# Optimization experiments

Measured on AMD Instinct MI355X. Metric: run time of the kernel, lower is better.

## Reference

```python
import jax, jax.numpy as jnp
import numpy as np

DIM, HEADS, DIM_HEAD = 1024, 16, 64
INNER = HEADS * DIM_HEAD  # 1024
FF = 4 * DIM
EPS = 1e-5


def layer_norm(x, g, b):
    mu = jnp.mean(x, axis=-1, keepdims=True)
    var = jnp.mean(jnp.square(x - mu), axis=-1, keepdims=True)
    return (x - mu) * jax.lax.rsqrt(var + EPS) * g + b


def setup_inputs() -> dict:
    key = jax.random.key(0)
    ks = jax.random.split(key, 8)
    B, N = 2, 2048
    s = 0.02
    return {
        "x": jax.random.normal(ks[0], (B, N, DIM), dtype=jnp.float32),
        "ln1_g": jnp.ones((DIM,), jnp.float32),
        "ln1_b": jnp.zeros((DIM,), jnp.float32),
        "ln2_g": jnp.ones((DIM,), jnp.float32),
        "ln2_b": jnp.zeros((DIM,), jnp.float32),
        "w_qkv": jax.random.normal(ks[1], (DIM, 3 * INNER), jnp.float32) * s,
        "w_out": jax.random.normal(ks[2], (INNER, DIM), jnp.float32) * s,
        "b_out": jnp.zeros((DIM,), jnp.float32),
        "w_ff1": jax.random.normal(ks[3], (DIM, FF), jnp.float32) * s,
        "b_ff1": jnp.zeros((FF,), jnp.float32),
        "w_ff2": jax.random.normal(ks[4], (FF, DIM), jnp.float32) * s,
        "b_ff2": jnp.zeros((DIM,), jnp.float32),
    }


def reference(x, ln1_g, ln1_b, ln2_g, ln2_b, w_qkv, w_out, b_out,
              w_ff1, b_ff1, w_ff2, b_ff2):
    B, N, _ = x.shape
    scale = DIM_HEAD ** -0.5
    h = layer_norm(x, ln1_g, ln1_b)
    qkv = h @ w_qkv  # [B, N, 3*INNER]
    q, k, v = jnp.split(qkv, 3, axis=-1)
    # b n (h d) -> b h n d
    def to_heads(t):
        return t.reshape(B, N, HEADS, DIM_HEAD).transpose(0, 2, 1, 3)
    q, k, v = to_heads(q), to_heads(k), to_heads(v)
    dots = jnp.einsum('bhnd,bhmd->bhnm', q, k) * scale
    attn = jax.nn.softmax(dots, axis=-1)  # dropout = identity (eval)
    out = jnp.einsum('bhnm,bhmd->bhnd', attn, v)
    out = out.transpose(0, 2, 1, 3).reshape(B, N, INNER)
    out = out @ w_out + b_out
    x = x + out  # residual
    h2 = layer_norm(x, ln2_g, ln2_b)
    ff = jax.nn.gelu(h2 @ w_ff1 + b_ff1, approximate=False) @ w_ff2 + b_ff2
    return x + ff
```

## Files before the change

kernel.cpp:

```cpp
#include <hip/hip_runtime.h>
#include <hip/hip_bf16.h>
#include <math.h>

#define SEQ   2048
#define BATCH 2
#define NROWS 4096
#define DIMM  1024
#define QKV3  3072
#define FFD   4096
#define NHEAD 16
#define DHEAD 64

typedef __bf16 bf16;
typedef __bf16 bf16x4 __attribute__((ext_vector_type(4)));
typedef __bf16 bf16x8 __attribute__((ext_vector_type(8)));
typedef float  f32x4  __attribute__((ext_vector_type(4)));

static __device__ __forceinline__ f32x4 mfma16(bf16x8 a, bf16x8 b, f32x4 c) {
    return __builtin_amdgcn_mfma_f32_16x16x32_bf16(a, b, c, 0, 0, 0);
}

#define GLDS16(gp, lp) __builtin_amdgcn_global_load_lds( \
    (__attribute__((address_space(1))) void*)(gp),       \
    (__attribute__((address_space(3))) void*)(lp), 16, 0, 0)

__global__ __launch_bounds__(256) void tcast_kernel(
    const float* __restrict__ src, bf16* __restrict__ dst, int K, int N)
{
    __shared__ float tile[32][33];
    const int n0 = blockIdx.x * 32;
    const int k0 = blockIdx.y * 32;
    const int r = threadIdx.x >> 5;
    const int c = threadIdx.x & 31;
    #pragma unroll
    for (int i = 0; i < 4; ++i)
        tile[r + 8 * i][c] = src[(size_t)(k0 + r + 8 * i) * N + n0 + c];
    __syncthreads();
    #pragma unroll
    for (int i = 0; i < 4; ++i)
        dst[(size_t)(n0 + r + 8 * i) * K + k0 + c] = (bf16)tile[c][r + 8 * i];
}

__global__ __launch_bounds__(256) void ln_cast_kernel(
    const float* __restrict__ x, const float* __restrict__ g,
    const float* __restrict__ b, bf16* __restrict__ out)
{
    const int row = blockIdx.x;
    const int t = threadIdx.x;
    const float4 v = ((const float4*)(x + (size_t)row * DIMM))[t];
    float s  = v.x + v.y + v.z + v.w;
    float sq = v.x * v.x + v.y * v.y + v.z * v.z + v.w * v.w;
    #pragma unroll
    for (int m = 1; m < 64; m <<= 1) {
        s  += __shfl_xor(s, m, 64);
        sq += __shfl_xor(sq, m, 64);
    }
    __shared__ float ss[4], ssq[4];
    const int wave = t >> 6;
    if ((t & 63) == 0) { ss[wave] = s; ssq[wave] = sq; }
    __syncthreads();
    s  = ss[0] + ss[1] + ss[2] + ss[3];
    sq = ssq[0] + ssq[1] + ssq[2] + ssq[3];
    const float mean = s * (1.0f / DIMM);
    const float var  = sq * (1.0f / DIMM) - mean * mean;
    const float rs   = rsqrtf(var + 1e-5f);
    const float4 gv = ((const float4*)g)[t];
    const float4 bv = ((const float4*)b)[t];
    bf16* o = out + (size_t)row * DIMM + t * 4;
    o[0] = (bf16)((v.x - mean) * rs * gv.x + bv.x);
    o[1] = (bf16)((v.y - mean) * rs * gv.y + bv.y);
    o[2] = (bf16)((v.z - mean) * rs * gv.z + bv.z);
    o[3] = (bf16)((v.w - mean) * rs * gv.w + bv.w);
}

template<int EPI>
__global__ __launch_bounds__(512, 2)
void gemm256_kernel(const bf16* __restrict__ A, const bf16* __restrict__ BT,
                    const float* __restrict__ bias, bf16* __restrict__ C,
                    int M, int N, int K, int ld)
{
    __shared__ bf16 As_[2][2][8192];
    __shared__ bf16 Bs_[2][2][8192];
    const int nb = N >> 8;
    const int chunk = (int)gridDim.x >> 3;
    const int idx = ((int)blockIdx.x & 7) * chunk + ((int)blockIdx.x >> 3);
    const int bm = idx / nb, bn = idx - bm * nb;
    const int tm = bm << 8, tn = bn << 8;
    const int tid = threadIdx.x;
    const int lane = tid & 63, w = tid >> 6;
    const int wr = w >> 2, wc = w & 3;
    const int lq = lane & 15, hk = lane >> 4;

    const int sr  = lane >> 3;
    const int sgo = (((lane & 7) ^ sr) << 3);
    const bf16* gA0 = A  + (size_t)(tm +       w * 8 + sr) * ld + sgo;
    const bf16* gA1 = A  + (size_t)(tm + 128 + w * 8 + sr) * ld + sgo;
    const bf16* gB0 = BT + (size_t)(tn +       w * 8 + sr) * ld + sgo;
    const bf16* gB1 = BT + (size_t)(tn + 128 + w * 8 + sr) * ld + sgo;
    const size_t l64 = (size_t)64 * ld;

#define STG(D, T) do {                                                   \
        const size_t ko_ = (size_t)(T) * 64;                             \
        GLDS16(gA0 + ko_,       &As_[D][0][w * 512]);                    \
        GLDS16(gA0 + ko_ + l64, &As_[D][0][4096 + w * 512]);             \
        GLDS16(gA1 + ko_,       &As_[D][1][w * 512]);                    \
        GLDS16(gA1 + ko_ + l64, &As_[D][1][4096 + w * 512]);             \
        GLDS16(gB0 + ko_,       &Bs_[D][0][w * 512]);                    \
        GLDS16(gB0 + ko_ + l64, &Bs_[D][0][4096 + w * 512]);             \
        GLDS16(gB1 + ko_,       &Bs_[D][1][w * 512]);                    \
        GLDS16(gB1 + ko_ + l64, &Bs_[D][1][4096 + w * 512]);             \
    } while (0)

    f32x4 acc[8][4] = {};

    const int NT = K >> 6;
    STG(0, 0);
    STG(1, 1);
    for (int t = 0; t < NT; ++t) {
        const int d = t & 1;
        if (t + 1 < NT) asm volatile("s_waitcnt vmcnt(8)" ::: "memory");
        else            asm volatile("s_waitcnt vmcnt(0)" ::: "memory");
        __builtin_amdgcn_s_barrier();

        const char* Ah = (const char*)&As_[d][wr][0];
        const char* Bh = (const char*)&Bs_[d][wc >> 1][0];

        bf16x8 bfv[4][2];
        #pragma unroll
        for (int nj = 0; nj < 4; ++nj) {
            const int lc = (wc & 1) * 64 + nj * 16 + lq;
            #pragma unroll
            for (int kk = 0; kk < 2; ++kk) {
                const int g = kk * 4 + hk;
                bfv[nj][kk] = *(const bf16x8*)(Bh + lc * 128 + ((g ^ (lc & 7)) << 4));
            }
        }
        #pragma unroll
        for (int half = 0; half < 2; ++half) {
            bf16x8 af[4][2];
            #pragma unroll
            for (int mi = 0; mi < 4; ++mi) {
                const int lr = (half * 4 + mi) * 16 + lq;
                #pragma unroll
                for (int kk = 0; kk < 2; ++kk) {
                    const int g = kk * 4 + hk;
                    af[mi][kk] = *(const bf16x8*)(Ah + lr * 128 + ((g ^ (lr & 7)) << 4));
                }
            }
            __builtin_amdgcn_s_setprio(1);
            #pragma unroll
            for (int mi = 0; mi < 4; ++mi)
                #pragma unroll
                for (int nj = 0; nj < 4; ++nj)
                    #pragma unroll
                    for (int kk = 0; kk < 2; ++kk)
                        acc[half * 4 + mi][nj] =
                            mfma16(bfv[nj][kk], af[mi][kk], acc[half * 4 + mi][nj]);
            __builtin_amdgcn_s_setprio(0);
        }

        asm volatile("" ::: "memory");
        __builtin_amdgcn_s_barrier();
        if (t + 2 < NT) STG(d, t + 2);
    }
#undef STG

    const int r0 = tm + wr * 128 + lq;
    const int c0 = tn + wc * 64 + (hk << 2);
    if (EPI == 0) {
        #pragma unroll
        for (int mi = 0; mi < 8; ++mi)
            #pragma unroll
            for (int nj = 0; nj < 4; ++nj) {
                bf16x4 pk = { (bf16)acc[mi][nj][0], (bf16)acc[mi][nj][1],
                              (bf16)acc[mi][nj][2], (bf16)acc[mi][nj][3] };
                *(bf16x4*)(C + (size_t)(r0 + mi * 16) * N + c0 + nj * 16) = pk;
            }
    } else {
        #pragma unroll
        for (int nj = 0; nj < 4; ++nj) {
            const float4 bv4 = *(const float4*)(bias + c0 + nj * 16);
            #pragma unroll
            for (int mi = 0; mi < 8; ++mi) {
                float v0 = acc[mi][nj][0] + bv4.x, v1 = acc[mi][nj][1] + bv4.y;
                float v2 = acc[mi][nj][2] + bv4.z, v3 = acc[mi][nj][3] + bv4.w;
                bf16x4 pk = {
                    (bf16)(0.5f * v0 * (1.0f + erff(v0 * 0.70710678118654752f))),
                    (bf16)(0.5f * v1 * (1.0f + erff(v1 * 0.70710678118654752f))),
                    (bf16)(0.5f * v2 * (1.0f + erff(v2 * 0.70710678118654752f))),
                    (bf16)(0.5f * v3 * (1.0f + erff(v3 * 0.70710678118654752f))) };
                *(bf16x4*)(C + (size_t)(r0 + mi * 16) * N + c0 + nj * 16) = pk;
            }
        }
    }
}

template<int EPI>
__global__ __launch_bounds__(256, 3)
void gemm_bt_kernel(const bf16* __restrict__ A, const bf16* __restrict__ BT,
                    const float* __restrict__ bias, const float* __restrict__ res,
                    void* __restrict__ Cout, int M, int N, int K, int ld)
{
    __shared__ bf16 As[3][4096];
    __shared__ bf16 Bs[3][4096];
    const int nb = N >> 7;
    const int chunk = (int)gridDim.x >> 3;
    int idx = (blockIdx.x & 7) * chunk + (blockIdx.x >> 3);
    int ks = 0;
    if (EPI == 3) {
        const int tiles = (M >> 7) * nb;
        ks = idx / tiles;
        idx -= ks * tiles;
    }
    const int bm = idx / nb, bn = idx - bm * nb;
    const int tm = bm << 7, tn = bn << 7;
    const int tid = threadIdx.x;
    const int lane = tid & 63, wave = tid >> 6;
    const int wm = (wave >> 1) << 6, wn = (wave & 1) << 6;
    const int kofs = ks * K;

    const bf16* ga = A  + (size_t)(tm + wave * 32 + (lane >> 2)) * ld + kofs + ((lane & 3) << 3);
    const bf16* gb = BT + (size_t)(tn + wave * 32 + (lane >> 2)) * ld + kofs + ((lane & 3) << 3);
    const size_t k16 = (size_t)16 * ld;

    f32x4 acc[4][4] = {};
    const int ro = (lane & 15) * 32 + ((lane >> 4) << 3);

#define GSTAGE(BUF, KO) do {                          \
        bf16* la_ = &As[BUF][wave * 1024];            \
        bf16* lb_ = &Bs[BUF][wave * 1024];            \
        GLDS16(ga + (KO),       la_);                 \
        GLDS16(ga + (KO) + k16, la_ + 512);           \
        GLDS16(gb + (KO),       lb_);                 \
        GLDS16(gb + (KO) + k16, lb_ + 512);           \
    } while (0)

    GSTAGE(0, 0);
    GSTAGE(1, 32);
    GSTAGE(2, 64);
    int cur = 0;
    for (int k0 = 0; k0 < K; k0 += 32) {
        if (k0 + 96 <= K)      asm volatile("s_waitcnt vmcnt(8)" ::: "memory");
        else if (k0 + 64 <= K) asm volatile("s_waitcnt vmcnt(4)" ::: "memory");
        else                   asm volatile("s_waitcnt vmcnt(0)" ::: "memory");
        __builtin_amdgcn_s_barrier();

        bf16x8 af[4], bfr[4];
        #pragma unroll
        for (int i = 0; i < 4; ++i) {
            af[i]  = *(const bf16x8*)(&As[cur][0] + (wm + i * 16) * 32 + ro);
            bfr[i] = *(const bf16x8*)(&Bs[cur][0] + (wn + i * 16) * 32 + ro);
        }
        #pragma unroll
        for (int i = 0; i < 4; ++i)
            #pragma unroll
            for (int j = 0; j < 4; ++j)
                acc[i][j] = mfma16(bfr[j], af[i], acc[i][j]);

        asm volatile("" ::: "memory");
        __builtin_amdgcn_s_barrier();
        asm volatile("" ::: "memory");
        if (k0 + 96 < K) GSTAGE(cur, k0 + 96);
        cur = (cur == 2) ? 0 : cur + 1;
    }
#undef GSTAGE

    const int lq = lane & 15, hk = lane >> 4;
    const int r0 = tm + wm + lq;
    const int c0 = tn + wn + (hk << 2);
    if (EPI == 1) {
        float* C = (float*)Cout;
        #pragma unroll
        for (int j = 0; j < 4; ++j) {
            const float4 bv4 = *(const float4*)(bias + c0 + j * 16);
            #pragma unroll
            for (int i = 0; i < 4; ++i) {
                const size_t off = (size_t)(r0 + i * 16) * N + c0 + j * 16;
                const float4 rv = *(const float4*)(res + off);
                float4 o;
                o.x = acc[i][j][0] + bv4.x + rv.x;
                o.y = acc[i][j][1] + bv4.y + rv.y;
                o.z = acc[i][j][2] + bv4.z + rv.z;
                o.w = acc[i][j][3] + bv4.w + rv.w;
                *(float4*)(C + off) = o;
            }
        }
    } else {
        float* C = (float*)(ks == 0 ? Cout : (void*)res);
        #pragma unroll
        for (int j = 0; j < 4; ++j)
            #pragma unroll
            for (int i = 0; i < 4; ++i) {
                float4 o = { acc[i][j][0], acc[i][j][1], acc[i][j][2], acc[i][j][3] };
                *(float4*)(C + (size_t)(r0 + i * 16) * N + c0 + j * 16) = o;
            }
    }
}

__global__ __launch_bounds__(256) void ff2_reduce_kernel(
    const float* __restrict__ p0, const float* __restrict__ p1,
    const float* __restrict__ bias, const float* __restrict__ res,
    float* __restrict__ out)
{
    const int i = blockIdx.x * 256 + threadIdx.x;
    const float4 a = ((const float4*)p0)[i];
    const float4 b = ((const float4*)p1)[i];
    const float4 r = ((const float4*)res)[i];
    const float4 g = ((const float4*)bias)[i & 255];
    float4 o;
    o.x = a.x + b.x + r.x + g.x;
    o.y = a.y + b.y + r.y + g.y;
    o.z = a.z + b.z + r.z + g.z;
    o.w = a.w + b.w + r.w + g.w;
    ((float4*)out)[i] = o;
}

__global__ __launch_bounds__(256) void vtrans_kernel(
    const bf16* __restrict__ qkv, bf16* __restrict__ vT)
{
    __shared__ bf16 t[64 * 64];
    const int n0 = blockIdx.x * 64;
    const int bh = blockIdx.y;
    const int b = bh >> 4, h = bh & 15;
    const bf16* src = qkv + (size_t)(b * SEQ + n0) * QKV3 + 2 * DIMM + h * DHEAD;

    #pragma unroll
    for (int it = 0; it < 2; ++it) {
        const int c = it * 256 + threadIdx.x;
        const int n = c >> 3, d8 = (c & 7) * 8;
        const bf16x8 v8 = *(const bf16x8*)(src + (size_t)n * QKV3 + d8);
        const int byte = (n * 128 + d8 * 2) ^ (((n >> 3) & 7) << 4);
        *(bf16x8*)((char*)t + byte) = v8;
    }
    __syncthreads();
    #pragma unroll
    for (int it = 0; it < 2; ++it) {
        const int c = it * 256 + threadIdx.x;
        const int d = c >> 3, nc = c & 7;
        bf16x8 o8;
        #pragma unroll
        for (int i = 0; i < 8; ++i) {
            const int n = nc * 8 + i;
            const int byte = (n * 128 + d * 2) ^ ((nc & 7) << 4);
            o8[i] = *(const bf16*)((const char*)t + byte);
        }
        *(bf16x8*)(vT + (size_t)bh * DHEAD * SEQ + (size_t)d * SEQ + n0 + nc * 8) = o8;
    }
}

__global__ __launch_bounds__(256, 4)
void attn_kernel(const bf16* __restrict__ qkv, const bf16* __restrict__ vT,
                 bf16* __restrict__ out)
{
    __shared__ bf16 Ks[2][64 * 64];
    __shared__ bf16 Vs[2][64 * 64];
    __shared__ bf16 Ps[4][16 * 64];
    const int bid = blockIdx.x;
    const int idx = (bid & 7) * 128 + (bid >> 3);
    const int qt = idx & 31;
    const int bh = idx >> 5;
    const int b = bh >> 4, h = bh & 15;
    const int tid = threadIdx.x;
    const int lane = tid & 63, wave = tid >> 6;
    const int q = lane & 15, hi = lane >> 4;

    const bf16* qbase = qkv + (size_t)(b * SEQ) * QKV3 + h * DHEAD;
    const bf16* kbase = qbase + DIMM;
    const bf16* vbase = vT + (size_t)bh * DHEAD * SEQ;

    const int q0 = qt * 64 + wave * 16;
    bf16x8 qf[2];
    {
        const bf16* qp = qbase + (size_t)(q0 + q) * QKV3 + (hi << 3);
        qf[0] = *(const bf16x8*)qp;
        qf[1] = *(const bf16x8*)(qp + 32);
        #pragma unroll
        for (int j = 0; j < 8; ++j) {
            qf[0][j] = (bf16)((float)qf[0][j] * 0.125f);
            qf[1][j] = (bf16)((float)qf[1][j] * 0.125f);
        }
    }

    const int srow = lane >> 3;
    const int scol = ((lane & 7) ^ srow) << 3;
    const bf16* gk = kbase + (size_t)(wave * 16 + srow) * QKV3 + scol;
    const bf16* gv = vbase + (size_t)(wave * 16 + srow) * SEQ + scol;

#define STAGE(BUF, KT) do {                                        \
        bf16* lk_ = &Ks[BUF][wave * 1024];                         \
        bf16* lv_ = &Vs[BUF][wave * 1024];                         \
        GLDS16(gk + (size_t)(KT) * QKV3,       lk_);               \
        GLDS16(gk + (size_t)((KT) + 8) * QKV3, lk_ + 512);         \
        GLDS16(gv + (KT),                      lv_);               \
        GLDS16(gv + (KT) + 8 * SEQ,            lv_ + 512);         \
    } while (0)

    float m = -1e30f, l = 0.0f;
    f32x4 o[4] = {};

    STAGE(0, 0);
    int cur = 0;
    for (int kt = 0; kt < SEQ; kt += 64) {
        __syncthreads();
        if (kt + 64 < SEQ) STAGE(cur ^ 1, kt + 64);

        f32x4 sv[4];
        __builtin_amdgcn_s_setprio(1);
        #pragma unroll
        for (int kf = 0; kf < 4; ++kf) {
            f32x4 z = {0.f, 0.f, 0.f, 0.f};
            sv[kf] = z;
            #pragma unroll
            for (int ks = 0; ks < 2; ++ks) {
                const int row = kf * 16 + q;
                const int bo = (row * 128 + ks * 64 + (hi << 4)) ^ ((row & 7) << 4);
                const bf16x8 kfrag = *(const bf16x8*)((const char*)&Ks[cur][0] + bo);
                sv[kf] = mfma16(kfrag, qf[ks], sv[kf]);
            }
        }
        __builtin_amdgcn_s_setprio(0);

        float pmax;
        {
            float a = fmaxf(fmaxf(sv[0][0], sv[0][1]), fmaxf(sv[0][2], sv[0][3]));
            float b2 = fmaxf(fmaxf(sv[1][0], sv[1][1]), fmaxf(sv[1][2], sv[1][3]));
            float c = fmaxf(fmaxf(sv[2][0], sv[2][1]), fmaxf(sv[2][2], sv[2][3]));
            float d = fmaxf(fmaxf(sv[3][0], sv[3][1]), fmaxf(sv[3][2], sv[3][3]));
            pmax = fmaxf(fmaxf(a, b2), fmaxf(c, d));
        }
        pmax = fmaxf(pmax, __shfl_xor(pmax, 16, 64));
        pmax = fmaxf(pmax, __shfl_xor(pmax, 32, 64));

        if (__any(pmax - m > 8.0f)) {
            const float nm = fmaxf(m, pmax);
            const float fr = __expf(m - nm);
            l *= fr;
            #pragma unroll
            for (int df = 0; df < 4; ++df) {
                o[df][0] *= fr; o[df][1] *= fr;
                o[df][2] *= fr; o[df][3] *= fr;
            }
            m = nm;
        }

        float rsum = 0.0f;
        #pragma unroll
        for (int kf = 0; kf < 4; ++kf) {
            float p0 = __expf(sv[kf][0] - m);
            float p1 = __expf(sv[kf][1] - m);
            float p2 = __expf(sv[kf][2] - m);
            float p3 = __expf(sv[kf][3] - m);
            rsum += (p0 + p1) + (p2 + p3);
            bf16x4 pk = { (bf16)p0, (bf16)p1, (bf16)p2, (bf16)p3 };
            const int bo = (q * 128 + kf * 32 + hi * 8) ^ ((q & 7) << 4);
            *(bf16x4*)((char*)Ps[wave] + bo) = pk;
        }
        rsum += __shfl_xor(rsum, 16, 64);
        rsum += __shfl_xor(rsum, 32, 64);
        l += rsum;

        bf16x8 pf[2];
        #pragma unroll
        for (int ks = 0; ks < 2; ++ks) {
            const int bo = (q * 128 + ks * 64 + (hi << 4)) ^ ((q & 7) << 4);
            pf[ks] = *(const bf16x8*)((const char*)Ps[wave] + bo);
        }
        __builtin_amdgcn_s_setprio(1);
        #pragma unroll
        for (int df = 0; df < 4; ++df)
            #pragma unroll
            for (int ks = 0; ks < 2; ++ks) {
                const int rowv = df * 16 + q;
                const int bo = (rowv * 128 + ks * 64 + (hi << 4)) ^ ((rowv & 7) << 4);
                const bf16x8 vfrag = *(const bf16x8*)((const char*)&Vs[cur][0] + bo);
                o[df] = mfma16(vfrag, pf[ks], o[df]);
            }
        __builtin_amdgcn_s_setprio(0);
        cur ^= 1;
    }
#undef STAGE

    {
        const float inv = 1.0f / l;
        const int grow = b * SEQ + q0 + q;
        #pragma unroll
        for (int df = 0; df < 4; ++df) {
            bf16x4 pk = { (bf16)(o[df][0] * inv), (bf16)(o[df][1] * inv),
                          (bf16)(o[df][2] * inv), (bf16)(o[df][3] * inv) };
            *(bf16x4*)(out + (size_t)grow * DIMM + h * DHEAD + df * 16 + hi * 4) = pk;
        }
    }
}

extern "C" void kernel_launch(void* const* d_in, const int* in_sizes, int n_in,
                              void* d_out, int out_size, void* d_ws, size_t ws_size,
                              hipStream_t stream)
{
    (void)in_sizes; (void)n_in; (void)out_size;
    const float* x    = (const float*)d_in[0];
    const float* ln1g = (const float*)d_in[1];
    const float* ln1b = (const float*)d_in[2];
    const float* ln2g = (const float*)d_in[3];
    const float* ln2b = (const float*)d_in[4];
    const float* wqkv = (const float*)d_in[5];
    const float* wout = (const float*)d_in[6];
    const float* bout = (const float*)d_in[7];
    const float* wff1 = (const float*)d_in[8];
    const float* bff1 = (const float*)d_in[9];
    const float* wff2 = (const float*)d_in[10];
    const float* bff2 = (const float*)d_in[11];

    char* ws = (char*)d_ws;
    const dim3 blk(256);
    const dim3 blk512(512);
    const bool splitk = ws_size >= 92274688ULL;

    if (splitk) {
        bf16*  wff2T = (bf16*)(ws);
        bf16*  woutT = (bf16*)(ws + 8388608);
        bf16*  wff1T = (bf16*)(ws + 10485760);
        bf16*  wqkvT = (bf16*)(ws + 18874368);
        bf16*  hbuf  = (bf16*)(ws + 25165824);
        bf16*  qkvb  = (bf16*)(ws + 33554432);
        bf16*  vT    = (bf16*)(ws + 58720256);
        bf16*  attnb = (bf16*)(ws + 67108864);
        float* x2    = (float*)(ws + 75497472);
        bf16*  fbuf  = (bf16*)(ws + 41943040);
        float* p0    = (float*)(ws + 8388608);
        float* p1    = (float*)(ws + 25165824);

        tcast_kernel<<<dim3(QKV3 / 32, DIMM / 32), blk, 0, stream>>>(wqkv, wqkvT, DIMM, QKV3);
        tcast_kernel<<<dim3(DIMM / 32, DIMM / 32), blk, 0, stream>>>(wout, woutT, DIMM, DIMM);
        tcast_kernel<<<dim3(FFD  / 32, DIMM / 32), blk, 0, stream>>>(wff1, wff1T, DIMM, FFD);
        tcast_kernel<<<dim3(DIMM / 32, FFD  / 32), blk, 0, stream>>>(wff2, wff2T, FFD, DIMM);

        ln_cast_kernel<<<NROWS, blk, 0, stream>>>(x, ln1g, ln1b, hbuf);
        gemm256_kernel<0><<<(NROWS / 256) * (QKV3 / 256), blk512, 0, stream>>>(
            hbuf, wqkvT, nullptr, qkvb, NROWS, QKV3, DIMM, DIMM);
        vtrans_kernel<<<dim3(SEQ / 64, BATCH * NHEAD), blk, 0, stream>>>(qkvb, vT);
        attn_kernel<<<dim3(1024), blk, 0, stream>>>(qkvb, vT, attnb);
        gemm_bt_kernel<1><<<(NROWS / 128) * (DIMM / 128), blk, 0, stream>>>(
            attnb, woutT, bout, x, x2, NROWS, DIMM, DIMM, DIMM);
        ln_cast_kernel<<<NROWS, blk, 0, stream>>>(x2, ln2g, ln2b, hbuf);
        gemm256_kernel<2><<<(NROWS / 256) * (FFD / 256), blk512, 0, stream>>>(
            hbuf, wff1T, bff1, fbuf, NROWS, FFD, DIMM, DIMM);
        gemm_bt_kernel<3><<<2 * (NROWS / 128) * (DIMM / 128), blk, 0, stream>>>(
            fbuf, wff2T, nullptr, (const float*)p1, p0, NROWS, DIMM, FFD / 2, FFD);
        ff2_reduce_kernel<<<(NROWS * DIMM) / 1024, blk, 0, stream>>>(
            p0, p1, bff2, x2, (float*)d_out);
    } else {
        bf16*  wqkvT = (bf16*)(ws);
        bf16*  woutT = (bf16*)(ws + 6291456);
        bf16*  wff1T = (bf16*)(ws + 8388608);
        bf16*  wff2T = (bf16*)(ws + 16777216);
        float* x2    = (float*)(ws + 25165824);
        bf16*  vT    = (bf16*)(ws + 25165824);
        bf16*  hbuf  = (bf16*)(ws + 41943040);
        bf16*  qkvb  = (bf16*)(ws + 50331648);
        bf16*  attnb = (bf16*)(ws + 75497472);
        bf16*  fbuf  = (bf16*)(ws + 50331648);

        tcast_kernel<<<dim3(QKV3 / 32, DIMM / 32), blk, 0, stream>>>(wqkv, wqkvT, DIMM, QKV3);
        tcast_kernel<<<dim3(DIMM / 32, DIMM / 32), blk, 0, stream>>>(wout, woutT, DIMM, DIMM);
        tcast_kernel<<<dim3(FFD  / 32, DIMM / 32), blk, 0, stream>>>(wff1, wff1T, DIMM, FFD);
        tcast_kernel<<<dim3(DIMM / 32, FFD  / 32), blk, 0, stream>>>(wff2, wff2T, FFD, DIMM);

        ln_cast_kernel<<<NROWS, blk, 0, stream>>>(x, ln1g, ln1b, hbuf);
        gemm256_kernel<0><<<(NROWS / 256) * (QKV3 / 256), blk512, 0, stream>>>(
            hbuf, wqkvT, nullptr, qkvb, NROWS, QKV3, DIMM, DIMM);
        vtrans_kernel<<<dim3(SEQ / 64, BATCH * NHEAD), blk, 0, stream>>>(qkvb, vT);
        attn_kernel<<<dim3(1024), blk, 0, stream>>>(qkvb, vT, attnb);
        gemm_bt_kernel<1><<<(NROWS / 128) * (DIMM / 128), blk, 0, stream>>>(
            attnb, woutT, bout, x, x2, NROWS, DIMM, DIMM, DIMM);
        ln_cast_kernel<<<NROWS, blk, 0, stream>>>(x2, ln2g, ln2b, hbuf);
        gemm256_kernel<2><<<(NROWS / 256) * (FFD / 256), blk512, 0, stream>>>(
            hbuf, wff1T, bff1, fbuf, NROWS, FFD, DIMM, DIMM);
        gemm_bt_kernel<1><<<(NROWS / 128) * (DIMM / 128), blk, 0, stream>>>(
            fbuf, wff2T, bff2, x2, (float*)d_out, NROWS, DIMM, FFD, FFD);
    }
}
```

Baseline: 271.0 us.

## Split 256x256 GEMM main loop into four quadrant phases with interleaved loads

```diff
diff --git a/kernel.cpp b/kernel.cpp
--- a/kernel.cpp
+++ b/kernel.cpp
@@ -23,6 +23,8 @@
 #define GLDS16(gp, lp) __builtin_amdgcn_global_load_lds( \
     (__attribute__((address_space(1))) void*)(gp),       \
     (__attribute__((address_space(3))) void*)(lp), 16, 0, 0)
+
+#define MEMFENCE asm volatile("" ::: "memory")
 
 __global__ __launch_bounds__(256) void tcast_kernel(
     const float* __restrict__ src, bf16* __restrict__ dst, int K, int N)
@@ -99,97 +101,129 @@
     const bf16* gB1 = BT + (size_t)(tn + 128 + w * 8 + sr) * ld + sgo;
     const size_t l64 = (size_t)64 * ld;
 
-#define STG(D, T) do {                                                   \
-        const size_t ko_ = (size_t)(T) * 64;                             \
-        GLDS16(gA0 + ko_,       &As_[D][0][w * 512]);                    \
-        GLDS16(gA0 + ko_ + l64, &As_[D][0][4096 + w * 512]);             \
-        GLDS16(gA1 + ko_,       &As_[D][1][w * 512]);                    \
-        GLDS16(gA1 + ko_ + l64, &As_[D][1][4096 + w * 512]);             \
-        GLDS16(gB0 + ko_,       &Bs_[D][0][w * 512]);                    \
-        GLDS16(gB0 + ko_ + l64, &Bs_[D][0][4096 + w * 512]);             \
-        GLDS16(gB1 + ko_,       &Bs_[D][1][w * 512]);                    \
-        GLDS16(gB1 + ko_ + l64, &Bs_[D][1][4096 + w * 512]);             \
-    } while (0)
+#define STG_A0(D, T) do { const size_t ko_ = (size_t)(T) * 64;              \
+        GLDS16(gA0 + ko_,       &As_[D][0][w * 512]);                       \
+        GLDS16(gA0 + ko_ + l64, &As_[D][0][4096 + w * 512]); } while (0)
+#define STG_A1(D, T) do { const size_t ko_ = (size_t)(T) * 64;              \
+        GLDS16(gA1 + ko_,       &As_[D][1][w * 512]);                       \
+        GLDS16(gA1 + ko_ + l64, &As_[D][1][4096 + w * 512]); } while (0)
+#define STG_B0(D, T) do { const size_t ko_ = (size_t)(T) * 64;              \
+        GLDS16(gB0 + ko_,       &Bs_[D][0][w * 512]);                       \
+        GLDS16(gB0 + ko_ + l64, &Bs_[D][0][4096 + w * 512]); } while (0)
+#define STG_B1(D, T) do { const size_t ko_ = (size_t)(T) * 64;              \
+        GLDS16(gB1 + ko_,       &Bs_[D][1][w * 512]);                       \
+        GLDS16(gB1 + ko_ + l64, &Bs_[D][1][4096 + w * 512]); } while (0)
 
     f32x4 acc[8][4] = {};
-
     const int NT = K >> 6;
-    STG(0, 0);
-    STG(1, 1);
+
+    STG_A0(0, 0); STG_B1(0, 0); STG_B0(0, 0); STG_A1(0, 0);
+    STG_B0(1, 1); STG_A1(1, 1);
+
     for (int t = 0; t < NT; ++t) {
-        const int d = t & 1;
-        if (t + 1 < NT) asm volatile("s_waitcnt vmcnt(8)" ::: "memory");
-        else            asm volatile("s_waitcnt vmcnt(0)" ::: "memory");
+        const int d = t & 1, e = d ^ 1;
+        if (t == NT - 1) asm volatile("s_waitcnt vmcnt(0)" ::: "memory");
+        else             asm volatile("s_waitcnt vmcnt(4)" ::: "memory");
         __builtin_amdgcn_s_barrier();
-
-        const char* Ah = (const char*)&As_[d][wr][0];
-        const char* Bh = (const char*)&Bs_[d][wc >> 1][0];
-
-        bf16x8 bfv[4][2];
-        #pragma unroll
-        for (int nj = 0; nj < 4; ++nj) {
-            const int lc = (wc & 1) * 64 + nj * 16 + lq;
-            #pragma unroll
-            for (int kk = 0; kk < 2; ++kk) {
-                const int g = kk * 4 + hk;
-                bfv[nj][kk] = *(const bf16x8*)(Bh + lc * 128 + ((g ^ (lc & 7)) << 4));
-            }
-        }
-        #pragma unroll
-        for (int half = 0; half < 2; ++half) {
-            bf16x8 af[4][2];
+        MEMFENCE;
+
+        const char* Ah0 = (const char*)&As_[d][0][0];
+        const char* Ah1 = (const char*)&As_[d][1][0];
+        const char* Bh0 = (const char*)&Bs_[d][0][0];
+        const char* Bh1 = (const char*)&Bs_[d][1][0];
+        bf16x8 af[4][2], bfv[2][2];
+
+#define DO_MFMA(MH, NH) do {                                                 \
+        __builtin_amdgcn_s_setprio(1);                                       \
+        _Pragma("unroll")                                                    \
+        for (int mi = 0; mi < 4; ++mi)                                       \
+            _Pragma("unroll")                                                \
+            for (int nj = 0; nj < 2; ++nj)                                   \
+                _Pragma("unroll")                                            \
+                for (int kk = 0; kk < 2; ++kk)                               \
+                    acc[(MH)*4+mi][(NH)*2+nj] =                              \
+                        mfma16(bfv[nj][kk], af[mi][kk], acc[(MH)*4+mi][(NH)*2+nj]); \
+        __builtin_amdgcn_s_setprio(0); } while (0)
+
+        {
             #pragma unroll
             for (int mi = 0; mi < 4; ++mi) {
-                const int lr = (half * 4 + mi) * 16 + lq;
-                #pragma unroll
-                for (int kk = 0; kk < 2; ++kk) {
-                    const int g = kk * 4 + hk;
-                    af[mi][kk] = *(const bf16x8*)(Ah + lr * 128 + ((g ^ (lr & 7)) << 4));
-                }
-            }
-            __builtin_amdgcn_s_setprio(1);
-            #pragma unroll
-            for (int mi = 0; mi < 4; ++mi)
-                #pragma unroll
-                for (int nj = 0; nj < 4; ++nj)
-                    #pragma unroll
-                    for (int kk = 0; kk < 2; ++kk)
-                        acc[half * 4 + mi][nj] =
-                            mfma16(bfv[nj][kk], af[mi][kk], acc[half * 4 + mi][nj]);
-            __builtin_amdgcn_s_setprio(0);
-        }
-
-        asm volatile("" ::: "memory");
-        __builtin_amdgcn_s_barrier();
-        if (t + 2 < NT) STG(d, t + 2);
-    }
-#undef STG
-
-    const int r0 = tm + wr * 128 + lq;
-    const int c0 = tn + wc * 64 + (hk << 2);
-    if (EPI == 0) {
-        #pragma unroll
-        for (int mi = 0; mi < 8; ++mi)
-            #pragma unroll
-            for (int nj = 0; nj < 4; ++nj) {
-                bf16x4 pk = { (bf16)acc[mi][nj][0], (bf16)acc[mi][nj][1],
-                              (bf16)acc[mi][nj][2], (bf16)acc[mi][nj][3] };
-                *(bf16x4*)(C + (size_t)(r0 + mi * 16) * N + c0 + nj * 16) = pk;
-            }
-    } else {
-        #pragma unroll
-        for (int nj = 0; nj < 4; ++nj) {
-            const float4 bv4 = *(const float4*)(bias + c0 + nj * 16);
-            #pragma unroll
-            for (int mi = 0; mi < 8; ++mi) {
-                float v0 = acc[mi][nj][0] + bv4.x, v1 = acc[mi][nj][1] + bv4.y;
-                float v2 = acc[mi][nj][2] + bv4.z, v3 = acc[mi][nj][3] + bv4.w;
+                const int lr = wr * 64 + mi * 16 + lq;
+                af[mi][0] = *(const bf16x8*)(Ah0 + lr * 128 + ((hk ^ (lr & 7)) << 4));
+                af[mi][1] = *(const bf16x8*)(Ah0 + lr * 128 + (((4 + hk) ^ (lr & 7)) << 4));
+            }
+            #pragma unroll
+            for (int nj = 0; nj < 2; ++nj) {
+                const int lc = wc * 32 + nj * 16 + lq;
+                bfv[nj][0] = *(const bf16x8*)(Bh0 + lc * 128 + ((hk ^ (lc & 7)) << 4));
+                bfv[nj][1] = *(const bf16x8*)(Bh0 + lc * 128 + (((4 + hk) ^ (lc & 7)) << 4));
+            }
+            if (t + 1 < NT) STG_A0(e, t + 1);
+            DO_MFMA(0, 0);
+        }
+        MEMFENCE; __builtin_amdgcn_s_barrier(); MEMFENCE;
+        {
+            #pragma unroll
+            for (int mi = 0; mi < 4; ++mi) {
+                const int lr = wr * 64 + mi * 16 + lq;
+                af[mi][0] = *(const bf16x8*)(Ah1 + lr * 128 + ((hk ^ (lr & 7)) << 4));
+                af[mi][1] = *(const bf16x8*)(Ah1 + lr * 128 + (((4 + hk) ^ (lr & 7)) << 4));
+            }
+            if (t + 1 < NT) STG_B1(e, t + 1);
+            DO_MFMA(1, 0);
+        }
+        MEMFENCE; __builtin_amdgcn_s_barrier(); MEMFENCE;
+        {
+            #pragma unroll
+            for (int nj = 0; nj < 2; ++nj) {
+                const int lc = wc * 32 + nj * 16 + lq;
+                bfv[nj][0] = *(const bf16x8*)(Bh1 + lc * 128 + ((hk ^ (lc & 7)) << 4));
+                bfv[nj][1] = *(const bf16x8*)(Bh1 + lc * 128 + (((4 + hk) ^ (lc & 7)) << 4));
+            }
+            if (t + 2 < NT) STG_B0(d, t + 2);
+            DO_MFMA(1, 1);
+        }
+        MEMFENCE; __builtin_amdgcn_s_barrier(); MEMFENCE;
+        {
+            #pragma unroll
+            for (int mi = 0; mi < 4; ++mi) {
+                const int lr = wr * 64 + mi * 16 + lq;
+                af[mi][0] = *(const bf16x8*)(Ah0 + lr * 128 + ((hk ^ (lr & 7)) << 4));
+                af[mi][1] = *(const bf16x8*)(Ah0 + lr * 128 + (((4 + hk) ^ (lr & 7)) << 4));
+            }
+            if (t + 2 < NT) STG_A1(d, t + 2);
+            DO_MFMA(0, 1);
+        }
+        MEMFENCE; __builtin_amdgcn_s_barrier(); MEMFENCE;
+#undef DO_MFMA
+    }
+#undef STG_A0
+#undef STG_A1
+#undef STG_B0
+#undef STG_B1
+
+    #pragma unroll
+    for (int i = 0; i < 8; ++i) {
+        const int mh = i >> 2, mi = i & 3;
+        const int row = tm + mh * 128 + wr * 64 + mi * 16 + lq;
+        #pragma unroll
+        for (int j = 0; j < 4; ++j) {
+            const int nh = j >> 1, nj = j & 1;
+            const int col = tn + nh * 128 + wc * 32 + nj * 16 + (hk << 2);
+            if (EPI == 0) {
+                bf16x4 pk = { (bf16)acc[i][j][0], (bf16)acc[i][j][1],
+                              (bf16)acc[i][j][2], (bf16)acc[i][j][3] };
+                *(bf16x4*)(C + (size_t)row * N + col) = pk;
+            } else {
+                const float4 bv4 = *(const float4*)(bias + col);
+                float v0 = acc[i][j][0] + bv4.x, v1 = acc[i][j][1] + bv4.y;
+                float v2 = acc[i][j][2] + bv4.z, v3 = acc[i][j][3] + bv4.w;
                 bf16x4 pk = {
                     (bf16)(0.5f * v0 * (1.0f + erff(v0 * 0.70710678118654752f))),
                     (bf16)(0.5f * v1 * (1.0f + erff(v1 * 0.70710678118654752f))),
                     (bf16)(0.5f * v2 * (1.0f + erff(v2 * 0.70710678118654752f))),
                     (bf16)(0.5f * v3 * (1.0f + erff(v3 * 0.70710678118654752f))) };
-                *(bf16x4*)(C + (size_t)(r0 + mi * 16) * N + c0 + nj * 16) = pk;
+                *(bf16x4*)(C + (size_t)row * N + col) = pk;
             }
         }
     }
@@ -257,9 +291,9 @@
             for (int j = 0; j < 4; ++j)
                 acc[i][j] = mfma16(bfr[j], af[i], acc[i][j]);
 
-        asm volatile("" ::: "memory");
+        MEMFENCE;
         __builtin_amdgcn_s_barrier();
-        asm volatile("" ::: "memory");
+        MEMFENCE;
         if (k0 + 96 < K) GSTAGE(cur, k0 + 96);
         cur = (cur == 2) ? 0 : cur + 1;
     }
```

Result: no change. 268.7 us (-0.9%).
